# Kernel optimization log

Measured on AMD Instinct MI355X. Metric: run time of the kernel, lower is better.

Reference implementation:

```python
import jax, jax.numpy as jnp
import numpy as np

EPS = 1e-5
N_POINTS = 262144
K_VOL = 27
N_PAIRS = 65536
C_IN = 64
C_OUT = 64


def setup_inputs() -> dict:
    key = jax.random.key(0)
    k1, k2, k3, k4 = jax.random.split(key, 4)
    std = 1.0 / np.sqrt(C_IN * K_VOL)  # matches reset_parameters uniform(-std, std)
    input_feat = jax.random.normal(k1, (N_POINTS, C_IN), dtype=jnp.float32)
    input_coord = jax.random.randint(k2, (N_POINTS, 4), 0, 1024, dtype=jnp.int32)
    input_cmap = jnp.arange(N_POINTS, dtype=jnp.int32)
    input_kmap = jax.random.randint(k3, (K_VOL, N_PAIRS, 2), 0, N_POINTS, dtype=jnp.int32)
    weight = jax.random.uniform(k4, (K_VOL, C_IN, C_OUT), dtype=jnp.float32,
                                minval=-std, maxval=std)
    bn_weight = jnp.ones((C_OUT,), dtype=jnp.float32)
    bn_bias = jnp.zeros((C_OUT,), dtype=jnp.float32)
    return {
        "input_feat": input_feat,
        "input_coord": input_coord,
        "input_cmap": input_cmap,
        "input_kmap": input_kmap,
        "weight": weight,
        "bn_weight": bn_weight,
        "bn_bias": bn_bias,
    }


def reference(input_feat, input_coord, input_cmap, input_kmap, weight, bn_weight, bn_bias):
    # Sparse 3D conv (stride=1 -> output coords == input coords) via
    # gather -> per-offset GEMM -> scatter-add, then training-mode BN + ReLU.
    n_out = input_feat.shape[0]
    in_idx = input_kmap[..., 0]   # [K, P]
    out_idx = input_kmap[..., 1]  # [K, P]
    gathered = input_feat[in_idx]                         # [K, P, Cin]
    partial = jnp.einsum('kpc,kcd->kpd', gathered, weight)  # [K, P, Cout]
    out = jax.ops.segment_sum(partial.reshape(-1, partial.shape[-1]),
                              out_idx.reshape(-1), num_segments=n_out)  # [N, Cout]
    # BatchNorm1d, training mode (batch statistics, biased variance)
    mean = jnp.mean(out, axis=0)
    var = jnp.var(out, axis=0)
    y = (out - mean) * jax.lax.rsqrt(var + EPS) * bn_weight + bn_bias
    return jax.nn.relu(y)
```

## Files before the change

kernel.cpp:

```cpp
#include <hip/hip_runtime.h>

#define NPTS 262144
#define KVOL 27
#define NPAIRS 65536
#define TP (KVOL*NPAIRS)
#define CH 64
#define NT32 (NPTS/32)
#define NSEG (NT32*32)
#define NBLK2 2048
#define MAXR 12

typedef __attribute__((ext_vector_type(8))) short bf16x8;
typedef __attribute__((ext_vector_type(4))) float f32x4;

__device__ inline unsigned short f2bf(float x){
  unsigned int u = __float_as_uint(x);
  u += 0x7FFFu + ((u >> 16) & 1u);
  return (unsigned short)(u >> 16);
}

__device__ inline bf16x8 pack8(float4 a, float4 b){
  bf16x8 r;
  r[0]=(short)f2bf(a.x); r[1]=(short)f2bf(a.y); r[2]=(short)f2bf(a.z); r[3]=(short)f2bf(a.w);
  r[4]=(short)f2bf(b.x); r[5]=(short)f2bf(b.y); r[6]=(short)f2bf(b.z); r[7]=(short)f2bf(b.w);
  return r;
}

template<bool BF16G>
__global__ void k_pre(const float* __restrict__ feat, const float* __restrict__ w,
                      const int2* __restrict__ km, unsigned short* __restrict__ featb,
                      unsigned short* __restrict__ wpack, int* __restrict__ cnt,
                      unsigned short* __restrict__ rankb){
  int i = blockIdx.x*256 + threadIdx.x;
  if (BF16G){
    float4 v = ((const float4*)feat)[i];
    ushort4 r;
    r.x = f2bf(v.x); r.y = f2bf(v.y); r.z = f2bf(v.z); r.w = f2bf(v.w);
    ((ushort4*)featb)[i] = r;
  }
  if (i < TP){
    int2 io = km[i];
    int k = i >> 16;
    int seg = ((io.y >> 5) << 5) | k;
    int rank = atomicAdd(&cnt[seg], 1);
    rankb[i] = (unsigned short)rank;
  }
  if (i < KVOL*CH*CH){
    int j = i & 7, col = (i >> 3) & 63, kb = (i >> 9) & 7, k = i >> 12;
    wpack[i] = f2bf(w[(k*CH + kb*8 + j)*CH + col]);
  }
}

__global__ void k_scan1(const int* __restrict__ cnt, int* __restrict__ loc, int* __restrict__ btot){
  int blk = blockIdx.x, t = threadIdx.x;
  int base = blk*2048 + t*8;
  int c[8]; int s = 0;
  #pragma unroll
  for (int i = 0; i < 8; i++){ c[i] = s; s += cnt[base+i]; }
  int l = t & 63;
  int v = s;
  #pragma unroll
  for (int d = 1; d < 64; d <<= 1){ int u = __shfl_up(v, d, 64); if (l >= d) v += u; }
  __shared__ int wt[4], wb[4];
  if (l == 63) wt[t>>6] = v;
  __syncthreads();
  if (t == 0){ int a = 0; for (int w = 0; w < 4; w++){ wb[w] = a; a += wt[w]; } }
  __syncthreads();
  int tb = wb[t>>6] + v - s;
  #pragma unroll
  for (int i = 0; i < 8; i++) loc[base+i] = tb + c[i];
  if (t == 255) btot[blk] = tb + s;
}

__global__ void k_scan2(const int* __restrict__ btot, int* __restrict__ bbase){
  __shared__ int sm_[128];
  int t = threadIdx.x;
  int mine = btot[t];
  sm_[t] = mine;
  __syncthreads();
  for (int d = 1; d < 128; d <<= 1){
    int v = (t >= d) ? sm_[t-d] : 0;
    __syncthreads();
    sm_[t] += v;
    __syncthreads();
  }
  bbase[t] = sm_[t] - mine;
}

__global__ void k_init(const int* __restrict__ loc, const int* __restrict__ cnt,
                       const int* __restrict__ bbase, int2* __restrict__ segd){
  int i = blockIdx.x*256 + threadIdx.x;
  segd[i] = make_int2(loc[i] + bbase[i >> 11], cnt[i]);
}

__global__ void k_scatter(const int2* __restrict__ km, const unsigned short* __restrict__ rankb,
                          const int2* __restrict__ segd, int* __restrict__ records){
  int i = blockIdx.x*256 + threadIdx.x;
  int2 io = km[i];
  int k = i >> 16;
  int seg = ((io.y >> 5) << 5) | k;
  int pos = segd[seg].x + rankb[i];
  records[pos] = io.x | ((io.y & 31) << 18);
}

template<bool BF16G>
__global__ __launch_bounds__(256, 4) void k_conv6(
    const unsigned short* __restrict__ featb, const float* __restrict__ featf,
    const unsigned short* __restrict__ wpack, const int* __restrict__ records,
    const int2* __restrict__ segd, float* __restrict__ out, float* __restrict__ partials)
{
  __shared__ int lcnt[4][32];
  __shared__ int lslot[4][MAXR*32];
  __shared__ float sred[4][2][64];

  int tid = threadIdx.x;
  int wv = tid>>6, l = tid&63, lg = l>>4, li = l&15;
  int t32 = blockIdx.x*4 + wv;
  int segbase = t32 << 5;

  const bf16x8* fb = (const bf16x8*)featb;
  const float4* ff = (const float4*)featf;
  const bf16x8* wbase = ((const bf16x8*)wpack) + lg*64 + li;

  f32x4 acc[2][4];
  #pragma unroll
  for (int rt = 0; rt < 2; rt++)
    #pragma unroll
    for (int ct = 0; ct < 4; ct++) acc[rt][ct] = (f32x4)(0.0f);

  int2 sd  = segd[segbase];
  int2 sd1 = segd[segbase + 1];
  int rec_pf = 0;
  if (l < sd.y) rec_pf = records[sd.x + l];

  for (int k = 0; k < KVOL; k++){
    int2 sd2 = segd[segbase + min(k + 2, 31)];
    int rec_nx = 0;
    if (l < sd1.y) rec_nx = records[sd1.x + l];

    int beg = sd.x, tot = sd.y;
    if (tot > 0){
      bf16x8 B[4][2];
      #pragma unroll
      for (int ct = 0; ct < 4; ct++)
        #pragma unroll
        for (int h = 0; h < 2; h++)
          B[ct][h] = wbase[k*512 + h*256 + ct*16];

      int rec = rec_pf;
      for (int c0 = 0; c0 < tot; c0 += 64){
        int cc = min(64, tot - c0);
        if (c0 > 0 && l < cc) rec = records[beg + c0 + l];
        if (l < 32) lcnt[wv][l] = 0;
        int rank = -1;
        if (l < cc){
          int slot = (rec >> 18) & 31;
          rank = atomicAdd(&lcnt[wv][slot], 1);
          if (rank < MAXR) lslot[wv][rank*32 + slot] = rec;
        }
        int cnt0 = min(lcnt[wv][li], MAXR);
        int cnt1 = min(lcnt[wv][16 + li], MAXR);
        for (int r = 0; r < MAXR; r++){
          int rec0 = lslot[wv][r*32 + li];
          int rec1 = lslot[wv][r*32 + 16 + li];
          bool v0 = (r < cnt0), v1 = (r < cnt1);
          unsigned long long b0 = __ballot(v0), b1 = __ballot(v1);
          bf16x8 A00 = (bf16x8)(short)0, A01 = (bf16x8)(short)0;
          bf16x8 A10 = (bf16x8)(short)0, A11 = (bf16x8)(short)0;
          if (v0){
            int in0 = rec0 & 0x3FFFF;
            if (BF16G){ A00 = fb[in0*8 + lg]; A01 = fb[in0*8 + 4 + lg]; }
            else {
              float4 u0 = ff[in0*16 + lg*2],     u1 = ff[in0*16 + lg*2 + 1];
              float4 u2 = ff[in0*16 + 8 + lg*2], u3 = ff[in0*16 + 8 + lg*2 + 1];
              A00 = pack8(u0, u1); A01 = pack8(u2, u3);
            }
          }
          if (v1){
            int in1 = rec1 & 0x3FFFF;
            if (BF16G){ A10 = fb[in1*8 + lg]; A11 = fb[in1*8 + 4 + lg]; }
            else {
              float4 u0 = ff[in1*16 + lg*2],     u1 = ff[in1*16 + lg*2 + 1];
              float4 u2 = ff[in1*16 + 8 + lg*2], u3 = ff[in1*16 + 8 + lg*2 + 1];
              A10 = pack8(u0, u1); A11 = pack8(u2, u3);
            }
          }
          if (b0){
            #pragma unroll
            for (int ct = 0; ct < 4; ct++){
              acc[0][ct] = __builtin_amdgcn_mfma_f32_16x16x32_bf16(A00, B[ct][0], acc[0][ct], 0, 0, 0);
              acc[0][ct] = __builtin_amdgcn_mfma_f32_16x16x32_bf16(A01, B[ct][1], acc[0][ct], 0, 0, 0);
            }
          }
          if (b1){
            #pragma unroll
            for (int ct = 0; ct < 4; ct++){
              acc[1][ct] = __builtin_amdgcn_mfma_f32_16x16x32_bf16(A10, B[ct][0], acc[1][ct], 0, 0, 0);
              acc[1][ct] = __builtin_amdgcn_mfma_f32_16x16x32_bf16(A11, B[ct][1], acc[1][ct], 0, 0, 0);
            }
          }
          if (__ballot(rank > r) == 0ull) break;
        }
      }
    }
    rec_pf = rec_nx; sd = sd1; sd1 = sd2;
  }

  #pragma unroll
  for (int rt = 0; rt < 2; rt++)
    #pragma unroll
    for (int r = 0; r < 4; r++){
      int row = t32*32 + rt*16 + lg*4 + r;
      #pragma unroll
      for (int ct = 0; ct < 4; ct++)
        out[row*CH + ct*16 + li] = acc[rt][ct][r];
    }

  float s1[4], s2[4];
  #pragma unroll
  for (int ct = 0; ct < 4; ct++){
    float a1 = 0.f, a2 = 0.f;
    #pragma unroll
    for (int rt = 0; rt < 2; rt++)
      #pragma unroll
      for (int r = 0; r < 4; r++){
        float v = acc[rt][ct][r];
        a1 += v; a2 += v*v;
      }
    a1 += __shfl_xor(a1, 16, 64); a1 += __shfl_xor(a1, 32, 64);
    a2 += __shfl_xor(a2, 16, 64); a2 += __shfl_xor(a2, 32, 64);
    s1[ct] = a1; s2[ct] = a2;
  }
  __syncthreads();
  if (l < 16){
    #pragma unroll
    for (int ct = 0; ct < 4; ct++){
      sred[wv][0][ct*16 + li] = s1[ct];
      sred[wv][1][ct*16 + li] = s2[ct];
    }
  }
  __syncthreads();
  if (tid < 128){
    int h = tid >> 6, c = tid & 63;
    float p = sred[0][h][c] + sred[1][h][c] + sred[2][h][c] + sred[3][h][c];
    partials[blockIdx.x*128 + tid] = p;
  }
}

__global__ void k_statred(const float* __restrict__ partials, float* __restrict__ stats){
  __shared__ float sm_[256];
  int c = blockIdx.x;
  int t = threadIdx.x;
  float s = 0.f;
  for (int b = t; b < NBLK2; b += 256) s += partials[b*128 + c];
  sm_[t] = s;
  __syncthreads();
  for (int d = 128; d > 0; d >>= 1){
    if (t < d) sm_[t] += sm_[t+d];
    __syncthreads();
  }
  if (t == 0) stats[c] = sm_[0];
}

__global__ void k_bn(float* __restrict__ out, const float* __restrict__ stats,
                     const float* __restrict__ g, const float* __restrict__ b){
  int i = blockIdx.x * blockDim.x + threadIdx.x;
  float4 v = ((const float4*)out)[i];
  int c0 = (i * 4) & 63;
  float vals[4] = {v.x, v.y, v.z, v.w};
  float res[4];
  #pragma unroll
  for (int q = 0; q < 4; q++){
    int c = c0 + q;
    float mean = stats[c] * (1.0f/NPTS);
    float var  = stats[64+c] * (1.0f/NPTS) - mean*mean;
    float inv  = rsqrtf(var + 1e-5f);
    float y = (vals[q] - mean) * inv * g[c] + b[c];
    res[q] = fmaxf(y, 0.0f);
  }
  float4 r; r.x=res[0]; r.y=res[1]; r.z=res[2]; r.w=res[3];
  ((float4*)out)[i] = r;
}

extern "C" void kernel_launch(void* const* d_in, const int* in_sizes, int n_in,
                              void* d_out, int out_size, void* d_ws, size_t ws_size,
                              hipStream_t stream) {
  const float* feat   = (const float*)d_in[0];
  const int*   kmap   = (const int*)d_in[3];
  const float* weight = (const float*)d_in[4];
  const float* bnw    = (const float*)d_in[5];
  const float* bnb    = (const float*)d_in[6];
  float* out = (float*)d_out;

  char* ws = (char*)d_ws;
  size_t cur = 0;
  auto take = [&](size_t bytes){
    cur = (cur + 255) & ~(size_t)255;
    size_t p = cur; cur += bytes; return p;
  };
  float* stats          = (float*)(ws + take(2*CH*sizeof(float)));
  float* partials       = (float*)(ws + take((size_t)NBLK2*128*sizeof(float)));
  int* cnt              = (int*)(ws + take((size_t)NSEG*4));
  int* loc              = (int*)(ws + take((size_t)NSEG*4));
  int2* segd            = (int2*)(ws + take((size_t)NSEG*8));
  int* btot             = (int*)(ws + take(128*4));
  int* bbase            = (int*)(ws + take(128*4));
  unsigned short* wpack = (unsigned short*)(ws + take((size_t)KVOL*CH*CH*2));
  unsigned short* rankb = (unsigned short*)(ws + take((size_t)TP*2));
  int* records          = (int*)(ws + take((size_t)TP*4));
  size_t featb_off      = take((size_t)NPTS*CH*2);
  bool useBf16 = (ws_size >= cur);
  unsigned short* featb = (unsigned short*)(ws + featb_off);

  hipMemsetAsync(cnt, 0, (size_t)NSEG*4, stream);

  const int2* km = (const int2*)kmap;
  if (useBf16)
    k_pre<true><<<NPTS*CH/4/256, 256, 0, stream>>>(feat, weight, km, featb, wpack, cnt, rankb);
  else
    k_pre<false><<<TP/256, 256, 0, stream>>>(feat, weight, km, featb, wpack, cnt, rankb);

  k_scan1<<<128, 256, 0, stream>>>(cnt, loc, btot);
  k_scan2<<<1, 128, 0, stream>>>(btot, bbase);
  k_init<<<NSEG/256, 256, 0, stream>>>(loc, cnt, bbase, segd);
  k_scatter<<<TP/256, 256, 0, stream>>>(km, rankb, segd, records);

  if (useBf16)
    k_conv6<true><<<NBLK2, 256, 0, stream>>>(featb, feat, wpack, records, segd, out, partials);
  else
    k_conv6<false><<<NBLK2, 256, 0, stream>>>(featb, feat, wpack, records, segd, out, partials);

  k_statred<<<128, 256, 0, stream>>>(partials, stats);
  k_bn<<<NPTS*CH/4/256, 256, 0, stream>>>(out, stats, bnw, bnb);
}
```

Baseline: 262.5 us.

## Replace three-kernel scan with atomic segment allocation and unroll gather loop by two

The exclusive scan over segment counts (scan1, scan2, init) becomes a single kernel that does a wave-level prefix sum and reserves a base offset with one global atomic per wave. Segment regions therefore land in arbitrary order, which is fine because each segment stores its own offset. The conv inner loop now uses a precomputed max row count per wave and handles two ranks per iteration, issuing both sets of feature gathers before the MFMAs to expose more memory-level parallelism. This costs more registers and may lower occupancy.

```diff
diff --git a/kernel.cpp b/kernel.cpp
--- a/kernel.cpp
+++ b/kernel.cpp
@@ -51,46 +51,19 @@
   }
 }
 
-__global__ void k_scan1(const int* __restrict__ cnt, int* __restrict__ loc, int* __restrict__ btot){
-  int blk = blockIdx.x, t = threadIdx.x;
-  int base = blk*2048 + t*8;
-  int c[8]; int s = 0;
-  #pragma unroll
-  for (int i = 0; i < 8; i++){ c[i] = s; s += cnt[base+i]; }
-  int l = t & 63;
-  int v = s;
+__global__ void k_assign(const int* __restrict__ cnt, int* __restrict__ gtot,
+                         int2* __restrict__ segd){
+  int i = blockIdx.x*256 + threadIdx.x;
+  int l = threadIdx.x & 63;
+  int c = cnt[i];
+  int v = c;
   #pragma unroll
   for (int d = 1; d < 64; d <<= 1){ int u = __shfl_up(v, d, 64); if (l >= d) v += u; }
-  __shared__ int wt[4], wb[4];
-  if (l == 63) wt[t>>6] = v;
-  __syncthreads();
-  if (t == 0){ int a = 0; for (int w = 0; w < 4; w++){ wb[w] = a; a += wt[w]; } }
-  __syncthreads();
-  int tb = wb[t>>6] + v - s;
-  #pragma unroll
-  for (int i = 0; i < 8; i++) loc[base+i] = tb + c[i];
-  if (t == 255) btot[blk] = tb + s;
-}
-
-__global__ void k_scan2(const int* __restrict__ btot, int* __restrict__ bbase){
-  __shared__ int sm_[128];
-  int t = threadIdx.x;
-  int mine = btot[t];
-  sm_[t] = mine;
-  __syncthreads();
-  for (int d = 1; d < 128; d <<= 1){
-    int v = (t >= d) ? sm_[t-d] : 0;
-    __syncthreads();
-    sm_[t] += v;
-    __syncthreads();
-  }
-  bbase[t] = sm_[t] - mine;
-}
-
-__global__ void k_init(const int* __restrict__ loc, const int* __restrict__ cnt,
-                       const int* __restrict__ bbase, int2* __restrict__ segd){
-  int i = blockIdx.x*256 + threadIdx.x;
-  segd[i] = make_int2(loc[i] + bbase[i >> 11], cnt[i]);
+  int wtot = __shfl(v, 63, 64);
+  int base = 0;
+  if (l == 63) base = atomicAdd(gtot, wtot);
+  base = __shfl(base, 63, 64);
+  segd[i] = make_int2(base + v - c, c);
 }
 
 __global__ void k_scatter(const int2* __restrict__ km, const unsigned short* __restrict__ rankb,
@@ -104,7 +77,7 @@
 }
 
 template<bool BF16G>
-__global__ __launch_bounds__(256, 4) void k_conv6(
+__global__ __launch_bounds__(256, 4) void k_conv8(
     const unsigned short* __restrict__ featb, const float* __restrict__ featf,
     const unsigned short* __restrict__ wpack, const int* __restrict__ records,
     const int2* __restrict__ segd, float* __restrict__ out, float* __restrict__ partials)
@@ -152,54 +125,94 @@
         int cc = min(64, tot - c0);
         if (c0 > 0 && l < cc) rec = records[beg + c0 + l];
         if (l < 32) lcnt[wv][l] = 0;
-        int rank = -1;
         if (l < cc){
           int slot = (rec >> 18) & 31;
-          rank = atomicAdd(&lcnt[wv][slot], 1);
+          int rank = atomicAdd(&lcnt[wv][slot], 1);
           if (rank < MAXR) lslot[wv][rank*32 + slot] = rec;
         }
         int cnt0 = min(lcnt[wv][li], MAXR);
         int cnt1 = min(lcnt[wv][16 + li], MAXR);
-        for (int r = 0; r < MAXR; r++){
-          int rec0 = lslot[wv][r*32 + li];
-          int rec1 = lslot[wv][r*32 + 16 + li];
-          bool v0 = (r < cnt0), v1 = (r < cnt1);
-          unsigned long long b0 = __ballot(v0), b1 = __ballot(v1);
-          bf16x8 A00 = (bf16x8)(short)0, A01 = (bf16x8)(short)0;
-          bf16x8 A10 = (bf16x8)(short)0, A11 = (bf16x8)(short)0;
-          if (v0){
-            int in0 = rec0 & 0x3FFFF;
-            if (BF16G){ A00 = fb[in0*8 + lg]; A01 = fb[in0*8 + 4 + lg]; }
+        int nr = max(cnt0, cnt1);
+        #pragma unroll
+        for (int d = 1; d < 16; d <<= 1) nr = max(nr, __shfl_xor(nr, d, 64));
+
+        for (int rb = 0; rb < nr; rb += 2){
+          int recA0 = lslot[wv][rb*32 + li];
+          int recA1 = lslot[wv][rb*32 + 16 + li];
+          int recB0 = lslot[wv][min(rb+1, MAXR-1)*32 + li];
+          int recB1 = lslot[wv][min(rb+1, MAXR-1)*32 + 16 + li];
+          bool vA0 = (rb < cnt0), vA1 = (rb < cnt1);
+          bool vB0 = (rb+1 < cnt0), vB1 = (rb+1 < cnt1);
+          bf16x8 a00 = (bf16x8)(short)0, a01 = (bf16x8)(short)0;
+          bf16x8 a10 = (bf16x8)(short)0, a11 = (bf16x8)(short)0;
+          bf16x8 b00 = (bf16x8)(short)0, b01 = (bf16x8)(short)0;
+          bf16x8 b10 = (bf16x8)(short)0, b11 = (bf16x8)(short)0;
+          if (vA0){
+            int in = recA0 & 0x3FFFF;
+            if (BF16G){ a00 = fb[in*8 + lg]; a01 = fb[in*8 + 4 + lg]; }
             else {
-              float4 u0 = ff[in0*16 + lg*2],     u1 = ff[in0*16 + lg*2 + 1];
-              float4 u2 = ff[in0*16 + 8 + lg*2], u3 = ff[in0*16 + 8 + lg*2 + 1];
-              A00 = pack8(u0, u1); A01 = pack8(u2, u3);
-            }
-          }
-          if (v1){
-            int in1 = rec1 & 0x3FFFF;
-            if (BF16G){ A10 = fb[in1*8 + lg]; A11 = fb[in1*8 + 4 + lg]; }
+              float4 u0 = ff[in*16 + lg*2],     u1 = ff[in*16 + lg*2 + 1];
+              float4 u2 = ff[in*16 + 8 + lg*2], u3 = ff[in*16 + 8 + lg*2 + 1];
+              a00 = pack8(u0, u1); a01 = pack8(u2, u3);
+            }
+          }
+          if (vA1){
+            int in = recA1 & 0x3FFFF;
+            if (BF16G){ a10 = fb[in*8 + lg]; a11 = fb[in*8 + 4 + lg]; }
             else {
-              float4 u0 = ff[in1*16 + lg*2],     u1 = ff[in1*16 + lg*2 + 1];
-              float4 u2 = ff[in1*16 + 8 + lg*2], u3 = ff[in1*16 + 8 + lg*2 + 1];
-              A10 = pack8(u0, u1); A11 = pack8(u2, u3);
-            }
-          }
-          if (b0){
+              float4 u0 = ff[in*16 + lg*2],     u1 = ff[in*16 + lg*2 + 1];
+              float4 u2 = ff[in*16 + 8 + lg*2], u3 = ff[in*16 + 8 + lg*2 + 1];
+              a10 = pack8(u0, u1); a11 = pack8(u2, u3);
+            }
+          }
+          if (vB0){
+            int in = recB0 & 0x3FFFF;
+            if (BF16G){ b00 = fb[in*8 + lg]; b01 = fb[in*8 + 4 + lg]; }
+            else {
+              float4 u0 = ff[in*16 + lg*2],     u1 = ff[in*16 + lg*2 + 1];
+              float4 u2 = ff[in*16 + 8 + lg*2], u3 = ff[in*16 + 8 + lg*2 + 1];
+              b00 = pack8(u0, u1); b01 = pack8(u2, u3);
+            }
+          }
+          if (vB1){
+            int in = recB1 & 0x3FFFF;
+            if (BF16G){ b10 = fb[in*8 + lg]; b11 = fb[in*8 + 4 + lg]; }
+            else {
+              float4 u0 = ff[in*16 + lg*2],     u1 = ff[in*16 + lg*2 + 1];
+              float4 u2 = ff[in*16 + 8 + lg*2], u3 = ff[in*16 + 8 + lg*2 + 1];
+              b10 = pack8(u0, u1); b11 = pack8(u2, u3);
+            }
+          }
+          if (__ballot(vA0)){
             #pragma unroll
             for (int ct = 0; ct < 4; ct++){
-              acc[0][ct] = __builtin_amdgcn_mfma_f32_16x16x32_bf16(A00, B[ct][0], acc[0][ct], 0, 0, 0);
-              acc[0][ct] = __builtin_amdgcn_mfma_f32_16x16x32_bf16(A01, B[ct][1], acc[0][ct], 0, 0, 0);
-            }
-          }
-          if (b1){
+              acc[0][ct] = __builtin_amdgcn_mfma_f32_16x16x32_bf16(a00, B[ct][0], acc[0][ct], 0, 0, 0);
+              acc[0][ct] = __builtin_amdgcn_mfma_f32_16x16x32_bf16(a01, B[ct][1], acc[0][ct], 0, 0, 0);
+            }
+          }
+          if (__ballot(vA1)){
             #pragma unroll
             for (int ct = 0; ct < 4; ct++){
-              acc[1][ct] = __builtin_amdgcn_mfma_f32_16x16x32_bf16(A10, B[ct][0], acc[1][ct], 0, 0, 0);
-              acc[1][ct] = __builtin_amdgcn_mfma_f32_16x16x32_bf16(A11, B[ct][1], acc[1][ct], 0, 0, 0);
-            }
-          }
-          if (__ballot(rank > r) == 0ull) break;
+              acc[1][ct] = __builtin_amdgcn_mfma_f32_16x16x32_bf16(a10, B[ct][0], acc[1][ct], 0, 0, 0);
+              acc[1][ct] = __builtin_amdgcn_mfma_f32_16x16x32_bf16(a11, B[ct][1], acc[1][ct], 0, 0, 0);
+            }
+          }
+          if (rb + 1 < nr){
+            if (__ballot(vB0)){
+              #pragma unroll
+              for (int ct = 0; ct < 4; ct++){
+                acc[0][ct] = __builtin_amdgcn_mfma_f32_16x16x32_bf16(b00, B[ct][0], acc[0][ct], 0, 0, 0);
+                acc[0][ct] = __builtin_amdgcn_mfma_f32_16x16x32_bf16(b01, B[ct][1], acc[0][ct], 0, 0, 0);
+              }
+            }
+            if (__ballot(vB1)){
+              #pragma unroll
+              for (int ct = 0; ct < 4; ct++){
+                acc[1][ct] = __builtin_amdgcn_mfma_f32_16x16x32_bf16(b10, B[ct][0], acc[1][ct], 0, 0, 0);
+                acc[1][ct] = __builtin_amdgcn_mfma_f32_16x16x32_bf16(b11, B[ct][1], acc[1][ct], 0, 0, 0);
+              }
+            }
+          }
         }
       }
     }
@@ -300,19 +313,17 @@
   };
   float* stats          = (float*)(ws + take(2*CH*sizeof(float)));
   float* partials       = (float*)(ws + take((size_t)NBLK2*128*sizeof(float)));
-  int* cnt              = (int*)(ws + take((size_t)NSEG*4));
-  int* loc              = (int*)(ws + take((size_t)NSEG*4));
+  int* cnt              = (int*)(ws + take((size_t)(NSEG+64)*4));
   int2* segd            = (int2*)(ws + take((size_t)NSEG*8));
-  int* btot             = (int*)(ws + take(128*4));
-  int* bbase            = (int*)(ws + take(128*4));
   unsigned short* wpack = (unsigned short*)(ws + take((size_t)KVOL*CH*CH*2));
   unsigned short* rankb = (unsigned short*)(ws + take((size_t)TP*2));
   int* records          = (int*)(ws + take((size_t)TP*4));
   size_t featb_off      = take((size_t)NPTS*CH*2);
   bool useBf16 = (ws_size >= cur);
   unsigned short* featb = (unsigned short*)(ws + featb_off);
-
-  hipMemsetAsync(cnt, 0, (size_t)NSEG*4, stream);
+  int* gtot = cnt + NSEG;
+
+  hipMemsetAsync(cnt, 0, (size_t)(NSEG+64)*4, stream);
 
   const int2* km = (const int2*)kmap;
   if (useBf16)
@@ -320,15 +331,13 @@
   else
     k_pre<false><<<TP/256, 256, 0, stream>>>(feat, weight, km, featb, wpack, cnt, rankb);
 
-  k_scan1<<<128, 256, 0, stream>>>(cnt, loc, btot);
-  k_scan2<<<1, 128, 0, stream>>>(btot, bbase);
-  k_init<<<NSEG/256, 256, 0, stream>>>(loc, cnt, bbase, segd);
+  k_assign<<<NSEG/256, 256, 0, stream>>>(cnt, gtot, segd);
   k_scatter<<<TP/256, 256, 0, stream>>>(km, rankb, segd, records);
 
   if (useBf16)
-    k_conv6<true><<<NBLK2, 256, 0, stream>>>(featb, feat, wpack, records, segd, out, partials);
+    k_conv8<true><<<NBLK2, 256, 0, stream>>>(featb, feat, wpack, records, segd, out, partials);
   else
-    k_conv6<false><<<NBLK2, 256, 0, stream>>>(featb, feat, wpack, records, segd, out, partials);
+    k_conv8<false><<<NBLK2, 256, 0, stream>>>(featb, feat, wpack, records, segd, out, partials);
 
   k_statred<<<128, 256, 0, stream>>>(partials, stats);
   k_bn<<<NPTS*CH/4/256, 256, 0, stream>>>(out, stats, bnw, bnb);
```

Result: slower. 315.1 us (+20.1%).
